# Kernel optimization log

Hardware: AMD Instinct MI355X
Metric: run time of the kernel (lower is better)

The kernel has to match this reference:

```python
import jax, jax.numpy as jnp
import numpy as np

B = 4096
V_ECC, V_ERR = 16, 12
T = 25
C_T = 32            # temporal_out
F_IN = C_T * T      # 800 = ChebConv in_channels
GCN_OUT = 64
HID2 = 256          # hidden_size * 2


def _ring_edge_index(n):
    # undirected ring (both directions), no self loops -- AHA-segment-style adjacency
    s = np.arange(n); t = (s + 1) % n
    return np.stack([np.concatenate([s, t]), np.concatenate([t, s])]).astype(np.int64)


def setup_inputs() -> dict:
    key = jax.random.key(0)
    ks = iter(jax.random.split(key, 24))
    p = lambda shape, sc=0.05: jax.random.normal(next(ks), shape, jnp.float32) * sc
    return {
        "ecc": jax.random.normal(next(ks), (B, V_ECC, T), jnp.float32),
        "err": jax.random.normal(next(ks), (B, V_ERR, T), jnp.float32),
        "conv_ecc_w": p((C_T, 1, 3)), "conv_ecc_b": p((C_T,)),
        "conv_err_w": p((C_T, 1, 3)), "conv_err_b": p((C_T,)),
        "cheb_ecc_W": p((2, F_IN, GCN_OUT)), "cheb_ecc_b": p((GCN_OUT,)),
        "cheb_err_W": p((2, F_IN, GCN_OUT)), "cheb_err_b": p((GCN_OUT,)),
        "ecc_proj_W": p((V_ECC * GCN_OUT, HID2)), "ecc_proj_b": p((HID2,)),
        "err_proj_W": p((V_ERR * GCN_OUT, HID2)), "err_proj_b": p((HID2,)),
        "attn_W": p((HID2, 1)), "attn_b": p((1,)),
        "fc2_W": p((HID2, 1)), "fc2_b": p((1,)),
        "edge_index_ecc": jnp.asarray(_ring_edge_index(V_ECC)),
        "edge_index_err": jnp.asarray(_ring_edge_index(V_ERR)),
    }


def _temporal_conv(x, w, b):
    # torch Conv1d(1, C_T, kernel=3, padding=1) applied per node, then
    # reshape(B, V, C_T*T) exactly like the torch code (channel-major per node).
    Bv, V, T_ = x.shape
    y = jax.lax.conv_general_dilated(x.reshape(Bv * V, 1, T_), w, (1,), [(1, 1)],
                                     dimension_numbers=("NCH", "OIH", "NCH"))
    y = y + b[None, :, None]
    return y.reshape(Bv, V, -1)  # [B, V, C_T*T]


def _cheb_conv(x, edge_index, W, b):
    # PyG ChebConv(K=2, normalization='sym', lambda_max=2.0):
    #   Lhat = 2 L / lambda_max - I = -D^{-1/2} A D^{-1/2}
    #   out  = Tx0 @ W[0] + Tx1 @ W[1] + b,  Tx0 = x, Tx1 = Lhat x
    # Batched over B with a single segment_sum (replaces the per-sample loop).
    src, dst = edge_index[0], edge_index[1]
    V = x.shape[1]
    deg = jax.ops.segment_sum(jnp.ones(src.shape, jnp.float32), src, num_segments=V)
    dis = jnp.where(deg > 0, jax.lax.rsqrt(jnp.maximum(deg, 1.0)), 0.0)
    w_e = -dis[src] * dis[dst]                        # [E]
    msg = x[:, src, :] * w_e[None, :, None]           # [B, E, F] gather
    Tx1 = jax.ops.segment_sum(msg.transpose(1, 0, 2), dst, num_segments=V)  # [V, B, F]
    Tx1 = Tx1.transpose(1, 0, 2)                      # [B, V, F] scatter-add
    return jnp.einsum("bvf,fo->bvo", x, W[0]) + jnp.einsum("bvf,fo->bvo", Tx1, W[1]) + b


def reference(ecc, err, conv_ecc_w, conv_ecc_b, conv_err_w, conv_err_b,
              cheb_ecc_W, cheb_ecc_b, cheb_err_W, cheb_err_b,
              ecc_proj_W, ecc_proj_b, err_proj_W, err_proj_b,
              attn_W, attn_b, fc2_W, fc2_b, edge_index_ecc, edge_index_err):
    Bv = ecc.shape[0]
    ecc_f = _temporal_conv(ecc, conv_ecc_w, conv_ecc_b)   # [B, 16, 800]
    err_f = _temporal_conv(err, conv_err_w, conv_err_b)   # [B, 12, 800]
    ecc_out = _cheb_conv(ecc_f, edge_index_ecc, cheb_ecc_W, cheb_ecc_b)  # [B, 16, 64]
    err_out = _cheb_conv(err_f, edge_index_err, cheb_err_W, cheb_err_b)  # [B, 12, 64]
    # gated fusion
    ecc_g = ecc_out.reshape(Bv, -1) @ ecc_proj_W + ecc_proj_b  # [B, 256]
    err_g = err_out.reshape(Bv, -1) @ err_proj_W + err_proj_b  # [B, 256]
    attn = jax.nn.sigmoid(jnp.tanh(ecc_g + err_g) @ attn_W + attn_b)  # [B, 1]
    fused = attn * ecc_g + (1.0 - attn) * err_g   # latent_layer (gated path skips fc1)
    x = jax.nn.relu(fused) @ fc2_W + fc2_b        # dropout = identity (eval mode)
    return jax.nn.sigmoid(x)                      # [B, 1]
```

## Files before the change

### kernel.cpp

```cpp
#include <hip/hip_runtime.h>
#include <hip/hip_bf16.h>
#include <math.h>


#define TM 16
#define HID2 256
#define KE 400
#define KR 300
#define CE 13
#define CR 10

#define OFF_A0   6400
#define OFF_B0   6656
#define OFF_CV   6912
#define KBF_ECC  7040
#define KBF_ERR  60288

typedef __attribute__((ext_vector_type(8))) short  short8;
typedef __attribute__((ext_vector_type(4))) float  f32x4;

static __device__ __forceinline__ float ldv(const void* p, int i, bool f32) {
    return f32 ? ((const float*)p)[i]
               : __bfloat162float(((const __hip_bfloat16*)p)[i]);
}

static __device__ __forceinline__ bool detect_f32(const void* ecc) {
    unsigned w = ((const unsigned*)ecc)[threadIdx.x & 63];
    int e0 = (w >> 7) & 0xff, e1 = (w >> 23) & 0xff;
    return __any((e0 >= 141) || (e1 >= 141)) != 0;
}

static __device__ __forceinline__ int bswz(int k, int o) {
    int c = k >> 5, q = (k >> 3) & 3, j = k & 7;
    int nt = o >> 4, li = o & 15;
    return (c * 16 + nt) * 512 + (q * 16 + li) * 8 + j;
}

static __device__ __forceinline__ unsigned pack_bf16(float x0, float x1) {
    __hip_bfloat16 h0 = __float2bfloat16(x0), h1 = __float2bfloat16(x1);
    unsigned u0 = *(unsigned short*)&h0, u1 = *(unsigned short*)&h1;
    return (u1 << 16) | u0;
}

__global__ void precompute1(const void* __restrict__ ecc,
                            const void* __restrict__ conv_ecc_w,
                            const void* __restrict__ conv_err_w,
                            const void* __restrict__ conv_ecc_b,
                            const void* __restrict__ conv_err_b,
                            const void* __restrict__ cheb_ecc_W,
                            const void* __restrict__ cheb_err_W,
                            float* __restrict__ ws) {
    bool f32 = detect_f32(ecc);
    int tid = threadIdx.x, o = tid & 63, cq = tid >> 6;
    __shared__ float s[256];
    if (blockIdx.x < 100) {
        int m = blockIdx.x / 25, tp = blockIdx.x % 25;
        const void* cw = (m < 2) ? conv_ecc_w : conv_err_w;
        const void* W  = (m < 2) ? cheb_ecc_W : cheb_err_W;
        int wofs = (m & 1) * (800 * 64);
        float acc = 0.f;
        for (int cc = 0; cc < 8; ++cc) {
            int c = cq * 8 + cc;
            #pragma unroll
            for (int k = 0; k < 3; ++k) {
                int t = tp + 1 - k;
                if (t >= 0 && t < 25)
                    acc += ldv(cw, c * 3 + k, f32) * ldv(W, wofs + (c * 25 + t) * 64 + o, f32);
            }
        }
        s[tid] = acc;
        __syncthreads();
        if (tid < 64)
            ws[m * 1600 + tp * 64 + o] = s[tid] + s[tid + 64] + s[tid + 128] + s[tid + 192];
    } else {
        int b = blockIdx.x - 100;
        int sig = b / 25, t = b % 25;
        const void* convb = sig ? conv_err_b : conv_ecc_b;
        const void* W     = sig ? cheb_err_W : cheb_ecc_W;
        float p = 0.f;
        for (int cc = 0; cc < 8; ++cc) {
            int c = cq * 8 + cc;
            float bc = ldv(convb, c, f32);
            p += bc * (ldv(W, (c * 25 + t) * 64 + o, f32)
                     - ldv(W, 800 * 64 + (c * 25 + t) * 64 + o, f32));
        }
        s[tid] = p;
        __syncthreads();
        if (tid < 64)
            atomicAdd(&ws[OFF_CV + sig * 64 + o],
                      s[tid] + s[tid + 64] + s[tid + 128] + s[tid + 192]);
    }
}

__global__ void precompute2(const void* __restrict__ ecc,
                            const void* __restrict__ ecc_proj_W,
                            const void* __restrict__ err_proj_W,
                            const void* __restrict__ ecc_proj_b,
                            const void* __restrict__ err_proj_b,
                            const void* __restrict__ cheb_ecc_b,
                            const void* __restrict__ cheb_err_b,
                            float* __restrict__ ws) {
    bool f32 = detect_f32(ecc);
    int tid = threadIdx.x;
    unsigned short* KbE = (unsigned short*)(ws + KBF_ECC);
    unsigned short* KbR = (unsigned short*)(ws + KBF_ERR);
    if (blockIdx.x < 700) {
        int row = blockIdx.x;
        int sig = (row >= KE);
        int lr  = sig ? row - KE : row;
        int v = lr / 25, tp = lr % 25;
        int V = sig ? 12 : 16;
        const void* P = sig ? err_proj_W : ecc_proj_W;
        const float* W0e = ws + (sig ? 3200 : 0)    + tp * 64;
        const float* W1e = ws + (sig ? 4800 : 1600) + tp * 64;
        __shared__ float w0_s[64], w1_s[64], part[512];
        if (tid < 64) { w0_s[tid] = W0e[tid]; w1_s[tid] = W1e[tid]; }
        __syncthreads();
        int o = tid & 255, jh = tid >> 8;
        int vp = (v + 1) % V, vm = (v + V - 1) % V;
        float acc = 0.f, s1 = 0.f;
        #pragma unroll 4
        for (int jj = 0; jj < 32; ++jj) {
            int j = jh * 32 + jj;
            acc += w0_s[j] * ldv(P, (v  * 64 + j) * HID2 + o, f32);
            s1  += w1_s[j] * (ldv(P, (vp * 64 + j) * HID2 + o, f32)
                            + ldv(P, (vm * 64 + j) * HID2 + o, f32));
        }
        part[tid] = acc - 0.5f * s1;
        __syncthreads();
        if (jh == 0) {
            float kval = part[o] + part[o + 256];
            __hip_bfloat16 h = __float2bfloat16(kval);
            (sig ? KbR : KbE)[bswz(lr, o)] = *(unsigned short*)&h;
        }
    } else if (blockIdx.x < 728) {
        int b = blockIdx.x - 700;
        int sig = (b >= 16);
        int v   = sig ? b - 16 : b;
        const void* P     = sig ? err_proj_W : ecc_proj_W;
        const void* chebb = sig ? cheb_err_b : cheb_ecc_b;
        const void* pb    = sig ? err_proj_b : ecc_proj_b;
        __shared__ float cv_s[64], part[512];
        if (tid < 64) cv_s[tid] = ldv(chebb, tid, f32) + ws[OFF_CV + sig * 64 + tid];
        __syncthreads();
        int o = tid & 255, jh = tid >> 8;
        float acc = 0.f;
        #pragma unroll 4
        for (int jj = 0; jj < 32; ++jj) {
            int j = jh * 32 + jj;
            acc += cv_s[j] * ldv(P, (v * 64 + j) * HID2 + o, f32);
        }
        part[tid] = acc;
        __syncthreads();
        if (jh == 0)
            atomicAdd(&ws[(sig ? OFF_B0 : OFF_A0) + o],
                      part[o] + part[o + 256] + ((v == 0) ? ldv(pb, o, f32) : 0.f));
    } else {
        for (int idx = tid; idx < (16 + 20) * 256; idx += 512) {
            if (idx < 16 * 256) KbE[bswz(400 + (idx >> 8), idx & 255)] = 0;
            else {
                int i2 = idx - 16 * 256;
                KbR[bswz(300 + (i2 >> 8), i2 & 255)] = 0;
            }
        }
    }
}

#define XR_DW 3328

__global__ __launch_bounds__(512, 2) void main_gemm(
        const void* __restrict__ ecc, const void* __restrict__ err,
        const void* __restrict__ attn_W, const void* __restrict__ attn_b,
        const void* __restrict__ fc2_W, const void* __restrict__ fc2_b,
        const float* __restrict__ ws, void* __restrict__ out) {
    __shared__ float smem[2 * 16 * 257];
    unsigned* xs = (unsigned*)smem;

    bool f32 = detect_f32(ecc);
    int tid  = threadIdx.x;
    int row0 = blockIdx.x * TM;

    for (int idx = tid; idx < 16 * 208; idx += 512) {
        int r = idx / 208, i2 = idx - r * 208;
        unsigned u = 0;
        if (i2 < 200) {
            if (f32) u = pack_bf16(((const float*)ecc)[(row0 + r) * 400 + 2 * i2],
                                   ((const float*)ecc)[(row0 + r) * 400 + 2 * i2 + 1]);
            else     u = ((const unsigned*)ecc)[(row0 + r) * 200 + i2];
        }
        xs[(i2 >> 4) * 256 + r * 16 + (i2 & 15)] = u;
    }
    for (int idx = tid; idx < 16 * 160; idx += 512) {
        int r = idx / 160, i2 = idx - r * 160;
        unsigned u = 0;
        if (i2 < 150) {
            if (f32) u = pack_bf16(((const float*)err)[(row0 + r) * 300 + 2 * i2],
                                   ((const float*)err)[(row0 + r) * 300 + 2 * i2 + 1]);
            else     u = ((const unsigned*)err)[(row0 + r) * 150 + i2];
        }
        xs[XR_DW + (i2 >> 4) * 256 + r * 16 + (i2 & 15)] = u;
    }
    __syncthreads();

    int wv = tid >> 6, lane = tid & 63;
    int m = lane & 15, quad = lane >> 4;
    int nt0 = wv * 2;

    const short8* KbE = (const short8*)(ws + KBF_ECC);
    const short8* KbR = (const short8*)(ws + KBF_ERR);
    const char* abase = (const char*)smem + m * 64 + quad * 16;

    f32x4 acc_e[2] = {{0.f, 0.f, 0.f, 0.f}, {0.f, 0.f, 0.f, 0.f}};
    f32x4 acc_r[2] = {{0.f, 0.f, 0.f, 0.f}, {0.f, 0.f, 0.f, 0.f}};

    #pragma unroll
    for (int c = 0; c < CE; ++c) {
        short8 a = *(const short8*)(abase + c * 1024);
        #pragma unroll
        for (int t = 0; t < 2; ++t)
            acc_e[t] = __builtin_amdgcn_mfma_f32_16x16x32_bf16(
                a, KbE[(c * 16 + nt0 + t) * 64 + lane], acc_e[t], 0, 0, 0);
    }
    #pragma unroll
    for (int c = 0; c < CR; ++c) {
        short8 a = *(const short8*)(abase + XR_DW * 4 + c * 1024);
        #pragma unroll
        for (int t = 0; t < 2; ++t)
            acc_r[t] = __builtin_amdgcn_mfma_f32_16x16x32_bf16(
                a, KbR[(c * 16 + nt0 + t) * 64 + lane], acc_r[t], 0, 0, 0);
    }
    __syncthreads();

    float* ge_s = smem;
    float* gr_s = smem + 16 * 257;
    #pragma unroll
    for (int t = 0; t < 2; ++t) {
        int col = (nt0 + t) * 16 + m;
        float a0v = ws[OFF_A0 + col], b0v = ws[OFF_B0 + col];
        #pragma unroll
        for (int i = 0; i < 4; ++i) {
            int row = quad * 4 + i;
            ge_s[row * 257 + col] = acc_e[t][i] + a0v;
            gr_s[row * 257 + col] = acc_r[t][i] + b0v;
        }
    }
    __syncthreads();

    float aw[4], fw[4];
    #pragma unroll
    for (int j = 0; j < 4; ++j) {
        aw[j] = ldv(attn_W, lane + 64 * j, f32);
        fw[j] = ldv(fc2_W,  lane + 64 * j, f32);
    }
    float ab = ldv(attn_b, 0, f32), fb = ldv(fc2_b, 0, f32);
    #pragma unroll
    for (int rr = 0; rr < 2; ++rr) {
        int r = wv * 2 + rr;
        float ge[4], gr[4];
        #pragma unroll
        for (int j = 0; j < 4; ++j) {
            ge[j] = ge_s[r * 257 + lane + 64 * j];
            gr[j] = gr_s[r * 257 + lane + 64 * j];
        }
        float p = 0.f;
        #pragma unroll
        for (int j = 0; j < 4; ++j) p += tanhf(ge[j] + gr[j]) * aw[j];
        #pragma unroll
        for (int off = 32; off; off >>= 1) p += __shfl_down(p, off);
        float a = 1.f / (1.f + expf(-(__shfl(p, 0) + ab)));
        float p2 = 0.f;
        #pragma unroll
        for (int j = 0; j < 4; ++j) {
            float fu = a * ge[j] + (1.f - a) * gr[j];
            p2 += fmaxf(fu, 0.f) * fw[j];
        }
        #pragma unroll
        for (int off = 32; off; off >>= 1) p2 += __shfl_down(p2, off);
        if (lane == 0) {
            float vout = 1.f / (1.f + expf(-(p2 + fb)));
            if (f32) ((float*)out)[row0 + r] = vout;
            else     ((__hip_bfloat16*)out)[row0 + r] = __float2bfloat16(vout);
        }
    }
}

extern "C" void kernel_launch(void* const* d_in, const int* in_sizes, int n_in,
                              void* d_out, int out_size, void* d_ws, size_t ws_size,
                              hipStream_t stream) {
    const void* ecc        = d_in[0];
    const void* err        = d_in[1];
    const void* conv_ecc_w = d_in[2];
    const void* conv_ecc_b = d_in[3];
    const void* conv_err_w = d_in[4];
    const void* conv_err_b = d_in[5];
    const void* cheb_ecc_W = d_in[6];
    const void* cheb_ecc_b = d_in[7];
    const void* cheb_err_W = d_in[8];
    const void* cheb_err_b = d_in[9];
    const void* ecc_proj_W = d_in[10];
    const void* ecc_proj_b = d_in[11];
    const void* err_proj_W = d_in[12];
    const void* err_proj_b = d_in[13];
    const void* attn_W     = d_in[14];
    const void* attn_b     = d_in[15];
    const void* fc2_W      = d_in[16];
    const void* fc2_b      = d_in[17];
    float* ws = (float*)d_ws;

    hipMemsetAsync((char*)d_ws + OFF_A0 * 4, 0, (256 + 256 + 128) * 4, stream);
    precompute1<<<150, 256, 0, stream>>>(ecc, conv_ecc_w, conv_err_w, conv_ecc_b,
                                         conv_err_b, cheb_ecc_W, cheb_err_W, ws);
    precompute2<<<729, 512, 0, stream>>>(ecc, ecc_proj_W, err_proj_W, ecc_proj_b,
                                         err_proj_b, cheb_ecc_b, cheb_err_b, ws);
    main_gemm<<<4096 / TM, 512, 0, stream>>>(ecc, err, attn_W, attn_b, fc2_W, fc2_b,
                                             ws, d_out);
}
```

Before: 130.4 us.

## Restructure weight-folding precompute kernels to reuse projection loads and drop atomics

The precompute2 kernel now computes all 25 time taps per (node, output-chunk) block. Each projection-weight load is reused across a time-tap vector held in shared memory, instead of one block per row reloading the projection weights 700 times. The bias reductions write per-part partial sums that are summed later, which removes the atomics and the memset launch. The zero-padding of the K tail moves into precompute1, and the workspace offsets shift to make room for the partial buffers. There are far fewer blocks, so each block does more serial work.

```diff
diff --git a/kernel.cpp b/kernel.cpp
--- a/kernel.cpp
+++ b/kernel.cpp
@@ -13,8 +13,8 @@
 #define OFF_A0   6400
 #define OFF_B0   6656
 #define OFF_CV   6912
-#define KBF_ECC  7040
-#define KBF_ERR  60288
+#define KBF_ECC  7424
+#define KBF_ERR  60672
 
 typedef __attribute__((ext_vector_type(8))) short  short8;
 typedef __attribute__((ext_vector_type(4))) float  f32x4;
@@ -42,7 +42,8 @@
     return (u1 << 16) | u0;
 }
 
-__global__ void precompute1(const void* __restrict__ ecc,
+__global__ __launch_bounds__(256) void precompute1(
+                            const void* __restrict__ ecc,
                             const void* __restrict__ conv_ecc_w,
                             const void* __restrict__ conv_err_w,
                             const void* __restrict__ conv_ecc_b,
@@ -72,27 +73,41 @@
         __syncthreads();
         if (tid < 64)
             ws[m * 1600 + tp * 64 + o] = s[tid] + s[tid + 64] + s[tid + 128] + s[tid + 192];
-    } else {
-        int b = blockIdx.x - 100;
-        int sig = b / 25, t = b % 25;
+    } else if (blockIdx.x < 108) {
+        int q = blockIdx.x - 100;
+        int sig = q >> 2, part = q & 3;
         const void* convb = sig ? conv_err_b : conv_ecc_b;
         const void* W     = sig ? cheb_err_W : cheb_ecc_W;
         float p = 0.f;
-        for (int cc = 0; cc < 8; ++cc) {
-            int c = cq * 8 + cc;
+        #pragma unroll
+        for (int cc = 0; cc < 2; ++cc) {
+            int c = part * 8 + cq * 2 + cc;
             float bc = ldv(convb, c, f32);
-            p += bc * (ldv(W, (c * 25 + t) * 64 + o, f32)
-                     - ldv(W, 800 * 64 + (c * 25 + t) * 64 + o, f32));
+            #pragma unroll 5
+            for (int t = 0; t < 25; ++t)
+                p += bc * (ldv(W, (c * 25 + t) * 64 + o, f32)
+                         - ldv(W, 800 * 64 + (c * 25 + t) * 64 + o, f32));
         }
         s[tid] = p;
         __syncthreads();
         if (tid < 64)
-            atomicAdd(&ws[OFF_CV + sig * 64 + o],
-                      s[tid] + s[tid + 64] + s[tid + 128] + s[tid + 192]);
-    }
-}
-
-__global__ void precompute2(const void* __restrict__ ecc,
+            ws[OFF_CV + (sig * 4 + part) * 64 + o] =
+                s[o] + s[o + 64] + s[o + 128] + s[o + 192];
+    } else {
+        unsigned short* KbE = (unsigned short*)(ws + KBF_ECC);
+        unsigned short* KbR = (unsigned short*)(ws + KBF_ERR);
+        for (int idx = tid; idx < (16 + 20) * 256; idx += 256) {
+            if (idx < 16 * 256) KbE[bswz(400 + (idx >> 8), idx & 255)] = 0;
+            else {
+                int i2 = idx - 16 * 256;
+                KbR[bswz(300 + (i2 >> 8), i2 & 255)] = 0;
+            }
+        }
+    }
+}
+
+__global__ __launch_bounds__(256) void precompute2(
+                            const void* __restrict__ ecc,
                             const void* __restrict__ ecc_proj_W,
                             const void* __restrict__ err_proj_W,
                             const void* __restrict__ ecc_proj_b,
@@ -101,68 +116,93 @@
                             const void* __restrict__ cheb_err_b,
                             float* __restrict__ ws) {
     bool f32 = detect_f32(ecc);
-    int tid = threadIdx.x;
-    unsigned short* KbE = (unsigned short*)(ws + KBF_ECC);
-    unsigned short* KbR = (unsigned short*)(ws + KBF_ERR);
-    if (blockIdx.x < 700) {
-        int row = blockIdx.x;
-        int sig = (row >= KE);
-        int lr  = sig ? row - KE : row;
-        int v = lr / 25, tp = lr % 25;
+    int tid = threadIdx.x, bid = blockIdx.x;
+    __shared__ f32x4 wt4[2][64][8];
+    __shared__ float red[256];
+    __shared__ float cv_s[64];
+
+    if (bid < 112) {
+        int sig = bid >= 64;
+        int lb  = sig ? bid - 64 : bid;
+        int v = lb >> 2, oc = lb & 3;
         int V = sig ? 12 : 16;
         const void* P = sig ? err_proj_W : ecc_proj_W;
-        const float* W0e = ws + (sig ? 3200 : 0)    + tp * 64;
-        const float* W1e = ws + (sig ? 4800 : 1600) + tp * 64;
-        __shared__ float w0_s[64], w1_s[64], part[512];
-        if (tid < 64) { w0_s[tid] = W0e[tid]; w1_s[tid] = W1e[tid]; }
-        __syncthreads();
-        int o = tid & 255, jh = tid >> 8;
-        int vp = (v + 1) % V, vm = (v + V - 1) % V;
-        float acc = 0.f, s1 = 0.f;
+        const float* wb0 = ws + (sig ? 3200 : 0);
+        const float* wb1 = ws + (sig ? 4800 : 1600);
+        float* wf = (float*)wt4;
+        f32x4 z = {0.f, 0.f, 0.f, 0.f};
+        for (int idx = tid; idx < 2 * 64 * 8; idx += 256)
+            ((f32x4*)wt4)[idx] = z;
+        __syncthreads();
+        for (int idx = tid; idx < 1600; idx += 256) {
+            int tp = idx >> 6, j = idx & 63;
+            wf[j * 32 + tp]        = wb0[idx];
+            wf[2048 + j * 32 + tp] = wb1[idx];
+        }
+        __syncthreads();
+
+        int ol = tid & 63, tpg = tid >> 6;
+        int o = oc * 64 + ol;
+        int vp1 = (v + 1) % V, vm1 = (v + V - 1) % V;
+        int b0 = v * 64 * HID2 + o, ba = vp1 * 64 * HID2 + o, bb = vm1 * 64 * HID2 + o;
+        f32x4 acc0 = z, acc1 = z;
         #pragma unroll 4
-        for (int jj = 0; jj < 32; ++jj) {
-            int j = jh * 32 + jj;
-            acc += w0_s[j] * ldv(P, (v  * 64 + j) * HID2 + o, f32);
-            s1  += w1_s[j] * (ldv(P, (vp * 64 + j) * HID2 + o, f32)
-                            + ldv(P, (vm * 64 + j) * HID2 + o, f32));
-        }
-        part[tid] = acc - 0.5f * s1;
-        __syncthreads();
-        if (jh == 0) {
-            float kval = part[o] + part[o + 256];
-            __hip_bfloat16 h = __float2bfloat16(kval);
-            (sig ? KbR : KbE)[bswz(lr, o)] = *(unsigned short*)&h;
-        }
-    } else if (blockIdx.x < 728) {
-        int b = blockIdx.x - 700;
-        int sig = (b >= 16);
-        int v   = sig ? b - 16 : b;
+        for (int j = 0; j < 64; ++j) {
+            float p0 = ldv(P, b0 + j * HID2, f32);
+            float pp = ldv(P, ba + j * HID2, f32) + ldv(P, bb + j * HID2, f32);
+            float ph = -0.5f * pp;
+            f32x4 w0a = wt4[0][j][tpg * 2], w0b = wt4[0][j][tpg * 2 + 1];
+            f32x4 w1a = wt4[1][j][tpg * 2], w1b = wt4[1][j][tpg * 2 + 1];
+            acc0 += w0a * p0 + w1a * ph;
+            acc1 += w0b * p0 + w1b * ph;
+        }
+        unsigned short* KB = (unsigned short*)(ws + (sig ? KBF_ERR : KBF_ECC));
+        #pragma unroll
+        for (int i = 0; i < 4; ++i) {
+            int tp = tpg * 8 + i;
+            if (tp < 25) {
+                __hip_bfloat16 h = __float2bfloat16(acc0[i]);
+                KB[bswz(v * 25 + tp, o)] = *(unsigned short*)&h;
+            }
+        }
+        #pragma unroll
+        for (int i = 0; i < 4; ++i) {
+            int tp = tpg * 8 + 4 + i;
+            if (tp < 25) {
+                __hip_bfloat16 h = __float2bfloat16(acc1[i]);
+                KB[bswz(v * 25 + tp, o)] = *(unsigned short*)&h;
+            }
+        }
+    } else {
+        int q = bid - 112;
+        int sig = q >> 2, oc = q & 3;
+        int V = sig ? 12 : 16, nv = V / 4;
         const void* P     = sig ? err_proj_W : ecc_proj_W;
         const void* chebb = sig ? cheb_err_b : cheb_ecc_b;
         const void* pb    = sig ? err_proj_b : ecc_proj_b;
-        __shared__ float cv_s[64], part[512];
-        if (tid < 64) cv_s[tid] = ldv(chebb, tid, f32) + ws[OFF_CV + sig * 64 + tid];
-        __syncthreads();
-        int o = tid & 255, jh = tid >> 8;
+        if (tid < 64) {
+            float c = ldv(chebb, tid, f32);
+            #pragma unroll
+            for (int p2 = 0; p2 < 4; ++p2)
+                c += ws[OFF_CV + (sig * 4 + p2) * 64 + tid];
+            cv_s[tid] = c;
+        }
+        __syncthreads();
+        int ol = tid & 63, vg = tid >> 6;
+        int o = oc * 64 + ol;
         float acc = 0.f;
-        #pragma unroll 4
-        for (int jj = 0; jj < 32; ++jj) {
-            int j = jh * 32 + jj;
-            acc += cv_s[j] * ldv(P, (v * 64 + j) * HID2 + o, f32);
-        }
-        part[tid] = acc;
-        __syncthreads();
-        if (jh == 0)
-            atomicAdd(&ws[(sig ? OFF_B0 : OFF_A0) + o],
-                      part[o] + part[o + 256] + ((v == 0) ? ldv(pb, o, f32) : 0.f));
-    } else {
-        for (int idx = tid; idx < (16 + 20) * 256; idx += 512) {
-            if (idx < 16 * 256) KbE[bswz(400 + (idx >> 8), idx & 255)] = 0;
-            else {
-                int i2 = idx - 16 * 256;
-                KbR[bswz(300 + (i2 >> 8), i2 & 255)] = 0;
-            }
-        }
+        for (int vv = 0; vv < nv; ++vv) {
+            int v = vg * nv + vv;
+            #pragma unroll 4
+            for (int j = 0; j < 64; ++j)
+                acc += cv_s[j] * ldv(P, (v * 64 + j) * HID2 + o, f32);
+        }
+        red[tid] = acc;
+        __syncthreads();
+        if (tid < 64)
+            ws[(sig ? OFF_B0 : OFF_A0) + oc * 64 + tid] =
+                red[tid] + red[tid + 64] + red[tid + 128] + red[tid + 192]
+                + ldv(pb, oc * 64 + tid, f32);
     }
 }
 
@@ -307,10 +347,9 @@
     const void* fc2_b      = d_in[17];
     float* ws = (float*)d_ws;
 
-    hipMemsetAsync((char*)d_ws + OFF_A0 * 4, 0, (256 + 256 + 128) * 4, stream);
-    precompute1<<<150, 256, 0, stream>>>(ecc, conv_ecc_w, conv_err_w, conv_ecc_b,
+    precompute1<<<109, 256, 0, stream>>>(ecc, conv_ecc_w, conv_err_w, conv_ecc_b,
                                          conv_err_b, cheb_ecc_W, cheb_err_W, ws);
-    precompute2<<<729, 512, 0, stream>>>(ecc, ecc_proj_W, err_proj_W, ecc_proj_b,
+    precompute2<<<120, 256, 0, stream>>>(ecc, ecc_proj_W, err_proj_W, ecc_proj_b,
                                          err_proj_b, cheb_ecc_b, cheb_err_b, ws);
     main_gemm<<<4096 / TM, 512, 0, stream>>>(ecc, err, attn_W, attn_b, fc2_W, fc2_b,
                                              ws, d_out);
```

Measured after the change: 139.1 us. 6.7% more time.

## Merge weight precompute kernels into one prep kernel, drop memset and atomics

Applied to the files above, without the earlier changes.

The two precompute kernels and the workspace memset are folded into a single prep launch. Each K-row block now computes its own folded conv·cheb weight vectors itself instead of reading them from a previous kernel. The bias blocks compute the bias contribution directly and write the final values without atomics. This removes two launches and a memset at the price of redundant per-block recomputation of small conv-weight products.

```diff
diff --git a/kernel.cpp b/kernel.cpp
--- a/kernel.cpp
+++ b/kernel.cpp
@@ -6,15 +6,14 @@
 #define TM 16
 #define HID2 256
 #define KE 400
-#define KR 300
 #define CE 13
 #define CR 10
 
 #define OFF_A0   6400
 #define OFF_B0   6656
-#define OFF_CV   6912
-#define KBF_ECC  7040
-#define KBF_ERR  60288
+#define KBF_ECC  7424
+#define KBF_ERR  60672
+#define XR_DW    3328
 
 typedef __attribute__((ext_vector_type(8))) short  short8;
 typedef __attribute__((ext_vector_type(4))) float  f32x4;
@@ -42,80 +41,54 @@
     return (u1 << 16) | u0;
 }
 
-__global__ void precompute1(const void* __restrict__ ecc,
-                            const void* __restrict__ conv_ecc_w,
-                            const void* __restrict__ conv_err_w,
-                            const void* __restrict__ conv_ecc_b,
-                            const void* __restrict__ conv_err_b,
-                            const void* __restrict__ cheb_ecc_W,
-                            const void* __restrict__ cheb_err_W,
-                            float* __restrict__ ws) {
+__global__ __launch_bounds__(512) void prep(
+        const void* __restrict__ ecc,
+        const void* __restrict__ conv_ecc_w, const void* __restrict__ conv_ecc_b,
+        const void* __restrict__ conv_err_w, const void* __restrict__ conv_err_b,
+        const void* __restrict__ cheb_ecc_W, const void* __restrict__ cheb_ecc_b,
+        const void* __restrict__ cheb_err_W, const void* __restrict__ cheb_err_b,
+        const void* __restrict__ ecc_proj_W, const void* __restrict__ ecc_proj_b,
+        const void* __restrict__ err_proj_W, const void* __restrict__ err_proj_b,
+        float* __restrict__ ws) {
     bool f32 = detect_f32(ecc);
-    int tid = threadIdx.x, o = tid & 63, cq = tid >> 6;
-    __shared__ float s[256];
-    if (blockIdx.x < 100) {
-        int m = blockIdx.x / 25, tp = blockIdx.x % 25;
-        const void* cw = (m < 2) ? conv_ecc_w : conv_err_w;
-        const void* W  = (m < 2) ? cheb_ecc_W : cheb_err_W;
-        int wofs = (m & 1) * (800 * 64);
-        float acc = 0.f;
-        for (int cc = 0; cc < 8; ++cc) {
-            int c = cq * 8 + cc;
-            #pragma unroll
-            for (int k = 0; k < 3; ++k) {
-                int t = tp + 1 - k;
-                if (t >= 0 && t < 25)
-                    acc += ldv(cw, c * 3 + k, f32) * ldv(W, wofs + (c * 25 + t) * 64 + o, f32);
-            }
-        }
-        s[tid] = acc;
-        __syncthreads();
-        if (tid < 64)
-            ws[m * 1600 + tp * 64 + o] = s[tid] + s[tid + 64] + s[tid + 128] + s[tid + 192];
-    } else {
-        int b = blockIdx.x - 100;
-        int sig = b / 25, t = b % 25;
-        const void* convb = sig ? conv_err_b : conv_ecc_b;
-        const void* W     = sig ? cheb_err_W : cheb_ecc_W;
-        float p = 0.f;
-        for (int cc = 0; cc < 8; ++cc) {
-            int c = cq * 8 + cc;
-            float bc = ldv(convb, c, f32);
-            p += bc * (ldv(W, (c * 25 + t) * 64 + o, f32)
-                     - ldv(W, 800 * 64 + (c * 25 + t) * 64 + o, f32));
-        }
-        s[tid] = p;
-        __syncthreads();
-        if (tid < 64)
-            atomicAdd(&ws[OFF_CV + sig * 64 + o],
-                      s[tid] + s[tid + 64] + s[tid + 128] + s[tid + 192]);
-    }
-}
-
-__global__ void precompute2(const void* __restrict__ ecc,
-                            const void* __restrict__ ecc_proj_W,
-                            const void* __restrict__ err_proj_W,
-                            const void* __restrict__ ecc_proj_b,
-                            const void* __restrict__ err_proj_b,
-                            const void* __restrict__ cheb_ecc_b,
-                            const void* __restrict__ cheb_err_b,
-                            float* __restrict__ ws) {
-    bool f32 = detect_f32(ecc);
-    int tid = threadIdx.x;
-    unsigned short* KbE = (unsigned short*)(ws + KBF_ECC);
-    unsigned short* KbR = (unsigned short*)(ws + KBF_ERR);
-    if (blockIdx.x < 700) {
-        int row = blockIdx.x;
-        int sig = (row >= KE);
-        int lr  = sig ? row - KE : row;
+    int tid = threadIdx.x, bid = blockIdx.x;
+    __shared__ float w0_s[64], w1_s[64], part[512];
+
+    if (bid < 700) {
+        int sig = bid >= KE;
+        int lr  = sig ? bid - KE : bid;
         int v = lr / 25, tp = lr % 25;
         int V = sig ? 12 : 16;
-        const void* P = sig ? err_proj_W : ecc_proj_W;
-        const float* W0e = ws + (sig ? 3200 : 0)    + tp * 64;
-        const float* W1e = ws + (sig ? 4800 : 1600) + tp * 64;
-        __shared__ float w0_s[64], w1_s[64], part[512];
-        if (tid < 64) { w0_s[tid] = W0e[tid]; w1_s[tid] = W1e[tid]; }
-        __syncthreads();
+        const void* P  = sig ? err_proj_W : ecc_proj_W;
+        const void* W  = sig ? cheb_err_W : cheb_ecc_W;
+        const void* cw = sig ? conv_err_w : conv_ecc_w;
+
+        {
+            int outp = tid >> 2, p = tid & 3;
+            int h = outp >> 6, j = outp & 63;
+            int wofs = h * 51200;
+            float a = 0.f;
+            #pragma unroll
+            for (int cc = 0; cc < 8; ++cc) {
+                int c = p * 8 + cc;
+                #pragma unroll
+                for (int k = 0; k < 3; ++k) {
+                    int t = tp + 1 - k;
+                    if (t >= 0 && t < 25)
+                        a += ldv(cw, c * 3 + k, f32)
+                           * ldv(W, wofs + (c * 25 + t) * 64 + j, f32);
+                }
+            }
+            part[tid] = a;
+        }
+        __syncthreads();
+        if (tid < 128) {
+            float s = part[tid * 4] + part[tid * 4 + 1]
+                    + part[tid * 4 + 2] + part[tid * 4 + 3];
+            if (tid < 64) w0_s[tid] = s; else w1_s[tid - 64] = s;
+        }
+        __syncthreads();
+
         int o = tid & 255, jh = tid >> 8;
         int vp = (v + 1) % V, vm = (v + V - 1) % V;
         float acc = 0.f, s1 = 0.f;
@@ -131,32 +104,66 @@
         if (jh == 0) {
             float kval = part[o] + part[o + 256];
             __hip_bfloat16 h = __float2bfloat16(kval);
-            (sig ? KbR : KbE)[bswz(lr, o)] = *(unsigned short*)&h;
-        }
-    } else if (blockIdx.x < 728) {
-        int b = blockIdx.x - 700;
-        int sig = (b >= 16);
-        int v   = sig ? b - 16 : b;
+            unsigned short* KB = (unsigned short*)(ws + (sig ? KBF_ERR : KBF_ECC));
+            KB[bswz(lr, o)] = *(unsigned short*)&h;
+        }
+    } else if (bid < 708) {
+        int q = bid - 700, sig = q >> 2, oc = q & 3;
+        int V = sig ? 12 : 16;
         const void* P     = sig ? err_proj_W : ecc_proj_W;
+        const void* W     = sig ? cheb_err_W : cheb_ecc_W;
+        const void* convb = sig ? conv_err_b : conv_ecc_b;
         const void* chebb = sig ? cheb_err_b : cheb_ecc_b;
         const void* pb    = sig ? err_proj_b : ecc_proj_b;
-        __shared__ float cv_s[64], part[512];
-        if (tid < 64) cv_s[tid] = ldv(chebb, tid, f32) + ws[OFF_CV + sig * 64 + tid];
-        __syncthreads();
-        int o = tid & 255, jh = tid >> 8;
+        __shared__ float cv_s[64];
+
+        {
+            int j = tid & 63, cp = tid >> 6;
+            float a = 0.f;
+            #pragma unroll
+            for (int cc = 0; cc < 4; ++cc) {
+                int c = cp * 4 + cc;
+                float bc = ldv(convb, c, f32);
+                float s = 0.f;
+                #pragma unroll 5
+                for (int t = 0; t < 25; ++t)
+                    s += ldv(W, (c * 25 + t) * 64 + j, f32)
+                       - ldv(W, 51200 + (c * 25 + t) * 64 + j, f32);
+                a += bc * s;
+            }
+            part[tid] = a;
+        }
+        __syncthreads();
+        if (tid < 64) {
+            float c = ldv(chebb, tid, f32);
+            #pragma unroll
+            for (int g = 0; g < 8; ++g) c += part[tid + 64 * g];
+            cv_s[tid] = c;
+        }
+        __syncthreads();
+
+        int ol = tid & 63, Jg = tid >> 6;
+        int o = oc * 64 + ol;
+        int JL = (V * 64) >> 3;
+        int Jb = Jg * JL;
         float acc = 0.f;
-        #pragma unroll 4
-        for (int jj = 0; jj < 32; ++jj) {
-            int j = jh * 32 + jj;
-            acc += cv_s[j] * ldv(P, (v * 64 + j) * HID2 + o, f32);
+        #pragma unroll 8
+        for (int jj = 0; jj < JL; ++jj) {
+            int J = Jb + jj;
+            acc += cv_s[J & 63] * ldv(P, J * HID2 + o, f32);
         }
         part[tid] = acc;
         __syncthreads();
-        if (jh == 0)
-            atomicAdd(&ws[(sig ? OFF_B0 : OFF_A0) + o],
-                      part[o] + part[o + 256] + ((v == 0) ? ldv(pb, o, f32) : 0.f));
+        if (tid < 64) {
+            float s = ldv(pb, oc * 64 + tid, f32);
+            #pragma unroll
+            for (int g = 0; g < 8; ++g) s += part[tid + 64 * g];
+            ws[(sig ? OFF_B0 : OFF_A0) + oc * 64 + tid] = s;
+        }
     } else {
-        for (int idx = tid; idx < (16 + 20) * 256; idx += 512) {
+        unsigned short* KbE = (unsigned short*)(ws + KBF_ECC);
+        unsigned short* KbR = (unsigned short*)(ws + KBF_ERR);
+        for (int idx = tid; idx < 36 * 256; idx += 512) {
             if (idx < 16 * 256) KbE[bswz(400 + (idx >> 8), idx & 255)] = 0;
             else {
                 int i2 = idx - 16 * 256;
@@ -165,8 +172,6 @@
         }
     }
 }
-
-#define XR_DW 3328
 
 __global__ __launch_bounds__(512, 2) void main_gemm(
         const void* __restrict__ ecc, const void* __restrict__ err,
@@ -307,11 +312,10 @@
     const void* fc2_b      = d_in[17];
     float* ws = (float*)d_ws;
 
-    hipMemsetAsync((char*)d_ws + OFF_A0 * 4, 0, (256 + 256 + 128) * 4, stream);
-    precompute1<<<150, 256, 0, stream>>>(ecc, conv_ecc_w, conv_err_w, conv_ecc_b,
-                                         conv_err_b, cheb_ecc_W, cheb_err_W, ws);
-    precompute2<<<729, 512, 0, stream>>>(ecc, ecc_proj_W, err_proj_W, ecc_proj_b,
-                                         err_proj_b, cheb_ecc_b, cheb_err_b, ws);
-    main_gemm<<<4096 / TM, 512, 0, stream>>>(ecc, err, attn_W, attn_b, fc2_W, fc2_b,
-                                             ws, d_out);
-}
+    prep<<<709, 512, 0, stream>>>(ecc, conv_ecc_w, conv_ecc_b, conv_err_w,
+                                  conv_err_b, cheb_ecc_W, cheb_ecc_b,
+                                  cheb_err_W, cheb_err_b, ecc_proj_W,
+                                  ecc_proj_b, err_proj_W, err_proj_b, ws);
+    main_gemm<<<4096 / TM, 512, 0, stream>>>(ecc, err, attn_W, attn_b, fc2_W,
+                                             fc2_b, ws, d_out);
+}
```

After: 130.8 us. About the same (+0.3%).
